# Kernel tuning notes

Measured on AMD Instinct MI355X. Metric: run time of the kernel, lower is better.

Reference implementation:

```python
import jax, jax.numpy as jnp
import numpy as np

ALPHA = 0.01  # LeakyReLU negative slope

def _leaky(x):
    return jnp.where(x > 0, x, ALPHA * x)

def _conv(x, w, b):
    # x: NHWC, w: HWIO, valid padding, stride 1
    return jax.lax.conv_general_dilated(x, w, (1, 1), 'VALID',
        dimension_numbers=('NHWC', 'HWIO', 'NHWC')) + b

def _maxpool2(x):
    return jax.lax.reduce_window(x, -jnp.inf, jax.lax.max,
        (1, 2, 2, 1), (1, 2, 2, 1), 'VALID')

def setup_inputs() -> dict:
    key = jax.random.key(0)
    ks = jax.random.split(key, 32)
    B, S, H = 32, 197, 256
    FLAT = 47 * 62 * 64  # after conv/pool trunk = 186496
    def w(k, shape, fan_in):
        return jax.random.normal(k, shape, dtype=jnp.float32) * np.float32(1.0 / np.sqrt(fan_in))
    inp = {
        'x': jax.random.normal(ks[0], (B, S, H), dtype=jnp.float32),
        'conv1_w': w(ks[1], (3, 3, 1, 32), 9), 'conv1_b': jnp.zeros((32,), jnp.float32),
        'conv2_w': w(ks[2], (3, 3, 32, 64), 288), 'conv2_b': jnp.zeros((64,), jnp.float32),
        'w_c1': w(ks[3], (FLAT, 512), FLAT), 'b_c1': jnp.zeros((512,), jnp.float32),
        'w_c2': w(ks[4], (512, 256), 512), 'b_c2': jnp.zeros((256,), jnp.float32),
        'w_co': w(ks[5], (256, 225 * 13), 256), 'b_co': jnp.zeros((225 * 13,), jnp.float32),
        'w_sm': w(ks[6], (13, 13), 13), 'b_sm': jnp.zeros((13,), jnp.float32),
        'w_r1': w(ks[7], (FLAT, 256), FLAT), 'b_r1': jnp.zeros((256,), jnp.float32),
        'w_r2': w(ks[8], (256, 128), 256), 'b_r2': jnp.zeros((128,), jnp.float32),
        'w_r3': w(ks[9], (128, 128), 128), 'b_r3': jnp.zeros((128,), jnp.float32),
        'w_r4': w(ks[10], (128, 64), 128), 'b_r4': jnp.zeros((64,), jnp.float32),
        'w_ro': w(ks[11], (64, 225 * 4), 64), 'b_ro': jnp.zeros((225 * 4,), jnp.float32),
        'w_sg': w(ks[12], (4, 4), 4), 'b_sg': jnp.zeros((4,), jnp.float32),
    }
    return inp

def reference(x, conv1_w, conv1_b, conv2_w, conv2_b,
              w_c1, b_c1, w_c2, b_c2, w_co, b_co, w_sm, b_sm,
              w_r1, b_r1, w_r2, b_r2, w_r3, b_r3, w_r4, b_r4,
              w_ro, b_ro, w_sg, b_sg):
    # CNN trunk on expanded hidden state (B, S, H, 1)
    h = x[..., None]
    h = jax.nn.relu(_conv(h, conv1_w, conv1_b))
    h = _maxpool2(h)
    h = jax.nn.relu(_conv(h, conv2_w, conv2_b))
    h = _maxpool2(h)
    h = h.reshape(h.shape[0], -1)  # (B, 186496)
    # classification branch (dropout is identity at inference)
    y = _leaky(h @ w_c1 + b_c1)
    y = _leaky(y @ w_c2 + b_c2)
    y = _leaky(y @ w_co + b_co).reshape(-1, 225, 13)
    # 225-step loop of shared Dense(13, softmax) heads -> one batched matmul
    class_out = jax.nn.softmax(jnp.einsum('bpi,ij->bpj', y, w_sm) + b_sm, axis=-1)
    z = _leaky(h @ w_r1 + b_r1)
    z = _leaky(z @ w_r2 + b_r2)
    z = _leaky(z @ w_r3 + b_r3)
    z = _leaky(z @ w_r4 + b_r4)
    z = (z @ w_ro + b_ro).reshape(-1, 225, 4)
    reg_out = jax.nn.sigmoid(jnp.einsum('bpi,ij->bpj', z, w_sg) + b_sg)
    return class_out, reg_out
```

## Files before the change

kernel.cpp:

```cpp
#include <hip/hip_runtime.h>
#include <hip/hip_bf16.h>

#define ALPHA 0.01f

typedef __attribute__((ext_vector_type(8))) __bf16 bf16x8;
typedef __attribute__((ext_vector_type(4))) float f32x4;

#define BATCH 32
#define P1H 97
#define P1W 127
#define P2W 62
#define FLAT 186496
#define GK 512
#define NGK 365
#define PSTRIDE1 16448
#define PSTRIDE2 8256
#define CONV1_BLOCKS 1540
#define LPITCH 264

#define BAR_LDS() asm volatile("s_waitcnt lgkmcnt(0)\n\ts_barrier" ::: "memory")

static __device__ __forceinline__ unsigned short f2bf(float x) {
  union { float f; unsigned u; } c; c.f = x;
  unsigned r = c.u + 0x7fffu + ((c.u >> 16) & 1u);
  return (unsigned short)(r >> 16);
}

static __device__ __forceinline__ unsigned pack2bf(float lo, float hi) {
  union { float f; unsigned u; } a, b;
  a.f = lo; b.f = hi;
  unsigned ra = (a.u + 0x7fffu + ((a.u >> 16) & 1u)) >> 16;
  unsigned rb = (b.u + 0x7fffu + ((b.u >> 16) & 1u)) & 0xffff0000u;
  return ra | rb;
}

__global__ __launch_bounds__(256) void conv1_pool(const float* __restrict__ x,
    const float* __restrict__ w1, const float* __restrict__ b1,
    unsigned short* __restrict__ p1,
    const float* __restrict__ w2, unsigned short* __restrict__ bpack) {
  if (blockIdx.x >= CONV1_BLOCKS) {
    int o = (blockIdx.x - CONV1_BLOCKS) * 256 + threadIdx.x;
    if (o < 9 * 4 * 512) {
      int f = o >> 9;
      int within = o & 511;
      int lane = within >> 3, j = within & 7;
      int tap = f >> 2, nf = f & 3;
      int k = ((lane >> 4) << 3) + j;
      int n = nf * 16 + (lane & 15);
      bpack[o] = f2bf(w2[(tap * 32 + k) * 64 + n]);
    }
    return;
  }
  int pid = blockIdx.x * 256 + threadIdx.x;
  if (pid >= BATCH * P1H * P1W) return;
  int b = pid / (P1H * P1W);
  int rem = pid - b * (P1H * P1W);
  int ph = rem / P1W;
  int pw = rem - ph * P1W;
  const float* xb = x + ((b * 197 + 2 * ph) * 256 + 2 * pw);
  float in[4][4];
#pragma unroll
  for (int r = 0; r < 4; ++r) {
    float2 v0 = *reinterpret_cast<const float2*>(xb + r * 256);
    float2 v1 = *reinterpret_cast<const float2*>(xb + r * 256 + 2);
    in[r][0] = v0.x; in[r][1] = v0.y; in[r][2] = v1.x; in[r][3] = v1.y;
  }
  unsigned pk[16];
#pragma unroll
  for (int c = 0; c < 32; ++c) {
    float s00 = b1[c], s01 = s00, s10 = s00, s11 = s00;
#pragma unroll
    for (int ky = 0; ky < 3; ++ky)
#pragma unroll
      for (int kx = 0; kx < 3; ++kx) {
        float w = w1[(ky * 3 + kx) * 32 + c];
        s00 = fmaf(in[ky][kx], w, s00);
        s01 = fmaf(in[ky][kx + 1], w, s01);
        s10 = fmaf(in[ky + 1][kx], w, s10);
        s11 = fmaf(in[ky + 1][kx + 1], w, s11);
      }
    float m = fmaxf(fmaxf(s00, s01), fmaxf(s10, s11));
    m = fmaxf(m, 0.0f);
    unsigned short u = f2bf(m);
    if (c & 1) pk[c >> 1] |= ((unsigned)u) << 16;
    else pk[c >> 1] = (unsigned)u;
  }
  uint4* dst = reinterpret_cast<uint4*>(p1 + (size_t)pid * 32);
#pragma unroll
  for (int g = 0; g < 4; ++g)
    dst[g] = make_uint4(pk[g * 4], pk[g * 4 + 1], pk[g * 4 + 2], pk[g * 4 + 3]);
}

__global__ __launch_bounds__(256) void conv2_pool(const unsigned short* __restrict__ p1,
    const unsigned short* __restrict__ bpack, const float* __restrict__ b2,
    unsigned short* __restrict__ hbf) {
  __shared__ alignas(16) unsigned char lds_buf[36864];
  int prow = blockIdx.x, b = blockIdx.y;
  int tid = threadIdx.x;
  int lane = tid & 63, wid = tid >> 6;
  {
    const uint4* src = reinterpret_cast<const uint4*>(bpack);
    uint4* dst = reinterpret_cast<uint4*>(lds_buf);
    for (int i = tid; i < 2304; i += 256) dst[i] = src[i];
  }
  __syncthreads();
  int row = lane & 15, kg = lane >> 4;
  int rowbase[4];
  int coff[4][3];
#pragma unroll
  for (int mf = 0; mf < 4; ++mf) {
    int m = wid * 64 + mf * 16 + row;
    int cro = m >> 7, cc = m & 127;
    rowbase[mf] = ((b * 97 + 2 * prow + cro) * 127) * 32 + kg * 8;
#pragma unroll
    for (int kx = 0; kx < 3; ++kx) {
      int ic = cc + kx; if (ic > 126) ic = 126;
      coff[mf][kx] = ic * 32;
    }
  }
  f32x4 acc[4][4];
#pragma unroll
  for (int i = 0; i < 4; ++i)
#pragma unroll
    for (int j = 0; j < 4; ++j) acc[i][j] = (f32x4){0.f, 0.f, 0.f, 0.f};

  const bf16x8* bl = reinterpret_cast<const bf16x8*>(lds_buf);
#pragma unroll
  for (int ky = 0; ky < 3; ++ky) {
#pragma unroll
    for (int kx = 0; kx < 3; ++kx) {
      int tap = ky * 3 + kx;
      bf16x8 a[4];
#pragma unroll
      for (int mf = 0; mf < 4; ++mf) {
        int addr = rowbase[mf] + ky * (127 * 32) + coff[mf][kx];
        a[mf] = *reinterpret_cast<const bf16x8*>(p1 + addr);
      }
      bf16x8 bf[4];
#pragma unroll
      for (int nf = 0; nf < 4; ++nf) bf[nf] = bl[(tap * 4 + nf) * 64 + lane];
#pragma unroll
      for (int nf = 0; nf < 4; ++nf)
#pragma unroll
        for (int mf = 0; mf < 4; ++mf)
          acc[mf][nf] = __builtin_amdgcn_mfma_f32_16x16x32_bf16(a[mf], bf[nf], acc[mf][nf], 0, 0, 0);
    }
  }
  __syncthreads();
  unsigned short* stage = reinterpret_cast<unsigned short*>(lds_buf);
#pragma unroll
  for (int mf = 0; mf < 4; ++mf)
#pragma unroll
    for (int nf = 0; nf < 4; ++nf) {
      int ch = nf * 16 + (lane & 15);
      float bias = b2[ch];
#pragma unroll
      for (int j = 0; j < 4; ++j) {
        int m = wid * 64 + mf * 16 + (lane >> 4) * 4 + j;
        float v = acc[mf][nf][j] + bias;
        stage[m * 64 + ch] = f2bf(fmaxf(v, 0.f));
      }
    }
  __syncthreads();
  unsigned short* hb = hbf + (size_t)b * FLAT + prow * (P2W * 64);
  for (int o = tid; o < P2W * 64; o += 256) {
    int pw = o >> 6, ch = o & 63;
    int c0 = 2 * pw;
    unsigned short v0 = stage[c0 * 64 + ch], v1 = stage[(c0 + 1) * 64 + ch];
    unsigned short v2 = stage[(128 + c0) * 64 + ch], v3 = stage[(129 + c0) * 64 + ch];
    unsigned short m01 = v0 > v1 ? v0 : v1;
    unsigned short m23 = v2 > v3 ? v2 : v3;
    hb[o] = m01 > m23 ? m01 : m23;
  }
}

__global__ __launch_bounds__(256) void gemm_mfma(
    const float* __restrict__ w_c1, const float* __restrict__ w_r1,
    const unsigned short* __restrict__ hbf,
    float* __restrict__ part1, float* __restrict__ part2) {
  __shared__ alignas(16) unsigned lds[16 * LPITCH];
  int py = blockIdx.x, kc = blockIdx.y;
  const float* W; int N, n0, cstride; float* pbase;
  if (py < 2) { W = w_c1; N = 512; n0 = py * 256; pbase = part1; cstride = PSTRIDE1; }
  else        { W = w_r1; N = 256; n0 = 0;        pbase = part2; cstride = PSTRIDE2; }
  int t = threadIdx.x, lane = t & 63, w = t >> 6;
  int k0 = kc * GK;
  int klen = FLAT - k0; if (klen > GK) klen = GK;
  int nsteps = klen >> 5;
  int cl = lane & 15, kg = lane >> 4;
  int mh = w & 1, nh = w >> 1;
  int kgl = kg & 1;

  const float* wsrc = W + (size_t)(k0 + w * 8) * N + n0 + lane * 4;
  unsigned* lwb = lds + (w * 4) * LPITCH + ((lane * 4) ^ ((w & 1) << 4));
  const unsigned short* ha = hbf + (size_t)(mh * 16 + cl) * FLAT + k0 + kg * 8;

  f32x4 acc[8];
#pragma unroll
  for (int f = 0; f < 8; ++f) acc[f] = (f32x4){0.f, 0.f, 0.f, 0.f};

  float4 st[8];
  bf16x8 a_cur, a_nxt;
  a_cur = *reinterpret_cast<const bf16x8*>(ha);
#pragma unroll
  for (int i = 0; i < 8; ++i)
    st[i] = *reinterpret_cast<const float4*>(wsrc + (size_t)i * N);

  for (int kt = 0; kt < nsteps; ++kt) {
    BAR_LDS();
#pragma unroll
    for (int ip = 0; ip < 4; ++ip) {
      float4 lo = st[2 * ip], hi = st[2 * ip + 1];
      *reinterpret_cast<uint4*>(lwb + ip * LPITCH) =
          make_uint4(pack2bf(lo.x, hi.x), pack2bf(lo.y, hi.y),
                     pack2bf(lo.z, hi.z), pack2bf(lo.w, hi.w));
    }
    if (kt + 1 < nsteps) {
      const float* ws = wsrc + (size_t)(kt + 1) * 32 * N;
#pragma unroll
      for (int i = 0; i < 8; ++i)
        st[i] = *reinterpret_cast<const float4*>(ws + (size_t)i * N);
    }
    BAR_LDS();
    if (kt + 1 < nsteps)
      a_nxt = *reinterpret_cast<const bf16x8*>(ha + (kt + 1) * 32);
#pragma unroll
    for (int f = 0; f < 8; ++f) {
      int col = nh * 128 + ((f ^ kgl) * 16) + cl;
      union { unsigned u[4]; bf16x8 v; } bb;
#pragma unroll
      for (int p = 0; p < 4; ++p)
        bb.u[p] = lds[(kg * 4 + p) * LPITCH + col];
      acc[f] = __builtin_amdgcn_mfma_f32_16x16x32_bf16(a_cur, bb.v, acc[f], 0, 0, 0);
    }
    a_cur = a_nxt;
  }

  float* out = pbase + (size_t)kc * cstride + n0;
#pragma unroll
  for (int f = 0; f < 8; ++f)
#pragma unroll
    for (int j = 0; j < 4; ++j) {
      int m = mh * 16 + kg * 4 + j;
      int col = nh * 128 + f * 16 + cl;
      out[m * N + col] = acc[f][j];
    }
}

__global__ __launch_bounds__(256) void reduce_big(const float* __restrict__ part1,
    const float* __restrict__ part2, const float* __restrict__ b_c1,
    const float* __restrict__ b_r1, float* __restrict__ y1, float* __restrict__ z1) {
  __shared__ float red[8][32];
  int b = blockIdx.x, t = threadIdx.x;
  int oo = t & 31, j = t >> 5;
  float s = 0.f;
  if (b < 512) {
    const float* p = part1 + b * 32 + oo;
    for (int c = j; c < NGK; c += 8) s += p[(size_t)c * PSTRIDE1];
    red[j][oo] = s;
    __syncthreads();
    if (t < 32) {
      float r = 0.f;
#pragma unroll
      for (int jj = 0; jj < 8; ++jj) r += red[jj][t];
      int o = b * 32 + t;
      r += b_c1[o & 511];
      y1[o] = r > 0.f ? r : ALPHA * r;
    }
  } else {
    const float* p = part2 + (b - 512) * 32 + oo;
    for (int c = j; c < NGK; c += 8) s += p[(size_t)c * PSTRIDE2];
    red[j][oo] = s;
    __syncthreads();
    if (t < 32) {
      float r = 0.f;
#pragma unroll
      for (int jj = 0; jj < 8; ++jj) r += red[jj][t];
      int u = (b - 512) * 32 + t;
      r += b_r1[u & 255];
      z1[u] = r > 0.f ? r : ALPHA * r;
    }
  }
}

__global__ __launch_bounds__(256) void tail_all(
    const float* __restrict__ y1g, const float* __restrict__ z1g,
    const float* __restrict__ w_c2, const float* __restrict__ b_c2,
    const float* __restrict__ w_co, const float* __restrict__ b_co,
    const float* __restrict__ w_sm, const float* __restrict__ b_sm,
    const float* __restrict__ w_r2, const float* __restrict__ b_r2,
    const float* __restrict__ w_r3, const float* __restrict__ b_r3,
    const float* __restrict__ w_r4, const float* __restrict__ b_r4,
    const float* __restrict__ w_ro, const float* __restrict__ b_ro,
    const float* __restrict__ w_sg, const float* __restrict__ b_sg,
    float* __restrict__ class_out, float* __restrict__ reg_out) {
  int tile = blockIdx.x, m = blockIdx.y, t = threadIdx.x;
  if (tile < 8) {
    __shared__ float ly1[512], ly2[256], ly3[29 * 13];
    ly1[t] = y1g[m * 512 + t];
    ly1[t + 256] = y1g[m * 512 + 256 + t];
    __syncthreads();
    {
      float s = b_c2[t];
      for (int k = 0; k < 512; ++k) s = fmaf(ly1[k], w_c2[k * 256 + t], s);
      ly2[t] = s > 0.f ? s : ALPHA * s;
    }
    __syncthreads();
    int p0 = tile * 29;
    int np = 225 - p0; if (np > 29) np = 29;
    int ncols = np * 13;
    for (int n = t; n < ncols; n += 256) {
      int col = p0 * 13 + n;
      float s = b_co[col];
      for (int k = 0; k < 256; ++k) s = fmaf(ly2[k], w_co[k * 2925 + col], s);
      ly3[n] = s > 0.f ? s : ALPHA * s;
    }
    __syncthreads();
    if (t < np) {
      float v[13], l[13], mx = -1e30f;
#pragma unroll
      for (int i = 0; i < 13; ++i) v[i] = ly3[t * 13 + i];
#pragma unroll
      for (int j = 0; j < 13; ++j) {
        float s = b_sm[j];
#pragma unroll
        for (int i = 0; i < 13; ++i) s = fmaf(v[i], w_sm[i * 13 + j], s);
        l[j] = s; mx = fmaxf(mx, s);
      }
      float sum = 0.f;
#pragma unroll
      for (int j = 0; j < 13; ++j) { l[j] = expf(l[j] - mx); sum += l[j]; }
      float inv = 1.f / sum;
      float* o = class_out + ((size_t)m * 225 + p0 + t) * 13;
#pragma unroll
      for (int j = 0; j < 13; ++j) o[j] = l[j] * inv;
    }
  } else {
    __shared__ float lz1[256], lz2[128], lz3[128], lz4[64], lzo[57 * 4];
    lz1[t] = z1g[m * 256 + t];
    __syncthreads();
    if (t < 128) {
      float s = b_r2[t];
      for (int k = 0; k < 256; ++k) s = fmaf(lz1[k], w_r2[k * 128 + t], s);
      lz2[t] = s > 0.f ? s : ALPHA * s;
    }
    __syncthreads();
    if (t < 128) {
      float s = b_r3[t];
      for (int k = 0; k < 128; ++k) s = fmaf(lz2[k], w_r3[k * 128 + t], s);
      lz3[t] = s > 0.f ? s : ALPHA * s;
    }
    __syncthreads();
    if (t < 64) {
      float s = b_r4[t];
      for (int k = 0; k < 128; ++k) s = fmaf(lz3[k], w_r4[k * 64 + t], s);
      lz4[t] = s > 0.f ? s : ALPHA * s;
    }
    __syncthreads();
    int p0 = (tile - 8) * 57;
    int np = 225 - p0; if (np > 57) np = 57;
    int ncols = np * 4;
    for (int n = t; n < ncols; n += 256) {
      int col = p0 * 4 + n;
      float s = b_ro[col];
#pragma unroll
      for (int k = 0; k < 64; ++k) s = fmaf(lz4[k], w_ro[k * 900 + col], s);
      lzo[n] = s;
    }
    __syncthreads();
    if (t < np) {
      float z[4];
#pragma unroll
      for (int i = 0; i < 4; ++i) z[i] = lzo[t * 4 + i];
      float* ro = reg_out + ((size_t)m * 225 + p0 + t) * 4;
#pragma unroll
      for (int j = 0; j < 4; ++j) {
        float s = b_sg[j];
#pragma unroll
        for (int i = 0; i < 4; ++i) s = fmaf(z[i], w_sg[i * 4 + j], s);
        ro[j] = 1.f / (1.f + expf(-s));
      }
    }
  }
}

#define OFF_P1     ((size_t)0)
#define OFF_BPACK  ((size_t)25229312)
#define OFF_H      ((size_t)25266176)
#define OFF_PART1  ((size_t)37201920)
#define OFF_PART2  ((size_t)61216000)
#define OFF_Y1     ((size_t)73269760)
#define OFF_Z1     ((size_t)73335296)

extern "C" void kernel_launch(void* const* d_in, const int* in_sizes, int n_in,
                              void* d_out, int out_size, void* d_ws, size_t ws_size,
                              hipStream_t stream) {
  const float* x     = (const float*)d_in[0];
  const float* w1    = (const float*)d_in[1];
  const float* b1    = (const float*)d_in[2];
  const float* w2    = (const float*)d_in[3];
  const float* b2    = (const float*)d_in[4];
  const float* w_c1  = (const float*)d_in[5];
  const float* b_c1  = (const float*)d_in[6];
  const float* w_c2  = (const float*)d_in[7];
  const float* b_c2  = (const float*)d_in[8];
  const float* w_co  = (const float*)d_in[9];
  const float* b_co  = (const float*)d_in[10];
  const float* w_sm  = (const float*)d_in[11];
  const float* b_sm  = (const float*)d_in[12];
  const float* w_r1  = (const float*)d_in[13];
  const float* b_r1  = (const float*)d_in[14];
  const float* w_r2  = (const float*)d_in[15];
  const float* b_r2  = (const float*)d_in[16];
  const float* w_r3  = (const float*)d_in[17];
  const float* b_r3  = (const float*)d_in[18];
  const float* w_r4  = (const float*)d_in[19];
  const float* b_r4  = (const float*)d_in[20];
  const float* w_ro  = (const float*)d_in[21];
  const float* b_ro  = (const float*)d_in[22];
  const float* w_sg  = (const float*)d_in[23];
  const float* b_sg  = (const float*)d_in[24];

  char* ws = (char*)d_ws;
  unsigned short* p1    = (unsigned short*)(ws + OFF_P1);
  unsigned short* bpack = (unsigned short*)(ws + OFF_BPACK);
  unsigned short* hbf   = (unsigned short*)(ws + OFF_H);
  float*          part1 = (float*)(ws + OFF_PART1);
  float*          part2 = (float*)(ws + OFF_PART2);
  float*          y1    = (float*)(ws + OFF_Y1);
  float*          z1    = (float*)(ws + OFF_Z1);

  float* class_out = (float*)d_out;
  float* reg_out   = (float*)d_out + 32 * 225 * 13;

  conv1_pool<<<CONV1_BLOCKS + 72, 256, 0, stream>>>(x, w1, b1, p1, w2, bpack);
  conv2_pool<<<dim3(47, 32), 256, 0, stream>>>(p1, bpack, b2, hbf);
  gemm_mfma<<<dim3(3, NGK), 256, 0, stream>>>(w_c1, w_r1, hbf, part1, part2);
  reduce_big<<<768, 256, 0, stream>>>(part1, part2, b_c1, b_r1, y1, z1);
  tail_all<<<dim3(12, 32), 256, 0, stream>>>(y1, z1,
      w_c2, b_c2, w_co, b_co, w_sm, b_sm,
      w_r2, b_r2, w_r3, b_r3, w_r4, b_r4,
      w_ro, b_ro, w_sg, b_sg, class_out, reg_out);
}
```

Measured before the change: 243.9 us.

## Double-buffer LDS in split-K GEMM and double the K chunk per block

```diff
diff --git a/kernel.cpp b/kernel.cpp
--- a/kernel.cpp
+++ b/kernel.cpp
@@ -11,8 +11,8 @@
 #define P1W 127
 #define P2W 62
 #define FLAT 186496
-#define GK 512
-#define NGK 365
+#define GK 1024
+#define NGK 183
 #define PSTRIDE1 16448
 #define PSTRIDE2 8256
 #define CONV1_BLOCKS 1540
@@ -178,7 +178,7 @@
     const float* __restrict__ w_c1, const float* __restrict__ w_r1,
     const unsigned short* __restrict__ hbf,
     float* __restrict__ part1, float* __restrict__ part2) {
-  __shared__ alignas(16) unsigned lds[16 * LPITCH];
+  __shared__ alignas(16) unsigned lds[2][16 * LPITCH];
   int py = blockIdx.x, kc = blockIdx.y;
   const float* W; int N, n0, cstride; float* pbase;
   if (py < 2) { W = w_c1; N = 512; n0 = py * 256; pbase = part1; cstride = PSTRIDE1; }
@@ -190,9 +190,10 @@
   int cl = lane & 15, kg = lane >> 4;
   int mh = w & 1, nh = w >> 1;
   int kgl = kg & 1;
+  size_t kstep = (size_t)32 * N;
 
   const float* wsrc = W + (size_t)(k0 + w * 8) * N + n0 + lane * 4;
-  unsigned* lwb = lds + (w * 4) * LPITCH + ((lane * 4) ^ ((w & 1) << 4));
+  int lwoff = (w * 4) * LPITCH + ((lane * 4) ^ ((w & 1) << 4));
   const unsigned short* ha = hbf + (size_t)(mh * 16 + cl) * FLAT + k0 + kg * 8;
 
   f32x4 acc[8];
@@ -200,40 +201,46 @@
   for (int f = 0; f < 8; ++f) acc[f] = (f32x4){0.f, 0.f, 0.f, 0.f};
 
   float4 st[8];
-  bf16x8 a_cur, a_nxt;
-  a_cur = *reinterpret_cast<const bf16x8*>(ha);
+  bf16x8 a_hold, a_next;
+  a_hold = *reinterpret_cast<const bf16x8*>(ha);
 #pragma unroll
   for (int i = 0; i < 8; ++i)
     st[i] = *reinterpret_cast<const float4*>(wsrc + (size_t)i * N);
 
-  for (int kt = 0; kt < nsteps; ++kt) {
+  for (int kt = 0; kt <= nsteps; ++kt) {
     BAR_LDS();
-#pragma unroll
-    for (int ip = 0; ip < 4; ++ip) {
-      float4 lo = st[2 * ip], hi = st[2 * ip + 1];
-      *reinterpret_cast<uint4*>(lwb + ip * LPITCH) =
-          make_uint4(pack2bf(lo.x, hi.x), pack2bf(lo.y, hi.y),
-                     pack2bf(lo.z, hi.z), pack2bf(lo.w, hi.w));
-    }
-    if (kt + 1 < nsteps) {
-      const float* ws = wsrc + (size_t)(kt + 1) * 32 * N;
-#pragma unroll
-      for (int i = 0; i < 8; ++i)
-        st[i] = *reinterpret_cast<const float4*>(ws + (size_t)i * N);
-    }
-    BAR_LDS();
-    if (kt + 1 < nsteps)
-      a_nxt = *reinterpret_cast<const bf16x8*>(ha + (kt + 1) * 32);
-#pragma unroll
-    for (int f = 0; f < 8; ++f) {
-      int col = nh * 128 + ((f ^ kgl) * 16) + cl;
-      union { unsigned u[4]; bf16x8 v; } bb;
-#pragma unroll
-      for (int p = 0; p < 4; ++p)
-        bb.u[p] = lds[(kg * 4 + p) * LPITCH + col];
-      acc[f] = __builtin_amdgcn_mfma_f32_16x16x32_bf16(a_cur, bb.v, acc[f], 0, 0, 0);
-    }
-    a_cur = a_nxt;
+    unsigned* wb = &lds[kt & 1][0] + lwoff;
+    if (kt < nsteps) {
+#pragma unroll
+      for (int ip = 0; ip < 4; ++ip) {
+        float4 lo = st[2 * ip], hi = st[2 * ip + 1];
+        *reinterpret_cast<uint4*>(wb + ip * LPITCH) =
+            make_uint4(pack2bf(lo.x, hi.x), pack2bf(lo.y, hi.y),
+                       pack2bf(lo.z, hi.z), pack2bf(lo.w, hi.w));
+      }
+      if (kt + 1 < nsteps) {
+        const float* ws = wsrc + (size_t)(kt + 1) * kstep;
+#pragma unroll
+        for (int i = 0; i < 8; ++i)
+          st[i] = *reinterpret_cast<const float4*>(ws + (size_t)i * N);
+      }
+    }
+    if (kt >= 1) {
+      a_next = a_hold;
+      if (kt < nsteps)
+        a_next = *reinterpret_cast<const bf16x8*>(ha + kt * 32);
+      const unsigned* rb = &lds[(kt - 1) & 1][0];
+#pragma unroll
+      for (int f = 0; f < 8; ++f) {
+        int col = nh * 128 + ((f ^ kgl) * 16) + cl;
+        union { unsigned u[4]; bf16x8 v; } bb;
+#pragma unroll
+        for (int p = 0; p < 4; ++p)
+          bb.u[p] = rb[(kg * 4 + p) * LPITCH + col];
+        acc[f] = __builtin_amdgcn_mfma_f32_16x16x32_bf16(a_hold, bb.v, acc[f], 0, 0, 0);
+      }
+      a_hold = a_next;
+    }
   }
 
   float* out = pbase + (size_t)kc * cstride + n0;
@@ -388,9 +395,9 @@
 #define OFF_BPACK  ((size_t)25229312)
 #define OFF_H      ((size_t)25266176)
 #define OFF_PART1  ((size_t)37201920)
-#define OFF_PART2  ((size_t)61216000)
-#define OFF_Y1     ((size_t)73269760)
-#define OFF_Z1     ((size_t)73335296)
+#define OFF_PART2  ((size_t)49241856)
+#define OFF_Y1     ((size_t)55285248)
+#define OFF_Z1     ((size_t)55350784)
 
 extern "C" void kernel_launch(void* const* d_in, const int* in_sizes, int n_in,
                               void* d_out, int out_size, void* d_ws, size_t ws_size,
```

After: 248.4 us. Within noise of the previous version (+1.8%).
